# Optimization experiments

Hardware: AMD Instinct MI355X
Metric: run time of the kernel (lower is better)

## Reference

```python
import jax, jax.numpy as jnp
from jax import lax
import numpy as np

DN = ('NHWC', 'HWIO', 'NHWC')  # NHWC activations, HWIO kernels (TF layout)
EPS = 1e-3


def setup_inputs() -> dict:
    key = jax.random.key(0)
    ks = jax.random.split(key, 6)
    B, H, W, C = 16, 64, 64, 256
    x = jax.random.normal(ks[0], (B, H, W, C), jnp.float32)
    # per-sample predicted kernels (scaled to keep activations well-conditioned)
    depthwise_kernels = jax.random.normal(ks[1], (B, 3, 3, C, C), jnp.float32) * 0.02
    pointwise_kernels = jax.random.normal(ks[2], (B, 1, 1, C, C), jnp.float32) * 0.06
    biases = jax.random.normal(ks[3], (B, C), jnp.float32) * 0.1
    # shared trailing Conv2D layer params
    conv_w = jax.random.normal(ks[4], (3, 3, C, C), jnp.float32) * 0.02
    conv_b = jnp.zeros((C,), jnp.float32)
    return dict(x=x, depthwise_kernels=depthwise_kernels,
                pointwise_kernels=pointwise_kernels, biases=biases,
                conv_w=conv_w, conv_b=conv_b)


def _instance_norm(x):
    # tf.nn.moments over spatial dims (population variance), eps=0.001
    mean = jnp.mean(x, axis=(1, 2), keepdims=True)
    var = jnp.var(x, axis=(1, 2), keepdims=True)
    return (x - mean) * lax.rsqrt(var + EPS)


def _reflect_pad_hw(x, p=1):
    pad = [(0, 0)] * (x.ndim - 3) + [(p, p), (p, p), (0, 0)]
    return jnp.pad(x, pad, mode='reflect')


def _per_sample_conv(xi, dk, pk, bi):
    # xi: [H,W,C]; dk: [3,3,C,Cm]; pk: [1,1,Cm,Co]; bi: [Co]
    xp = _reflect_pad_hw(xi)[None]  # [1,H+2,W+2,C]
    y = lax.conv_general_dilated(xp, dk, (1, 1), 'VALID', dimension_numbers=DN)
    y = lax.conv_general_dilated(y, pk, (1, 1), 'VALID', dimension_numbers=DN)
    return (y + bi)[0]


def reference(x, depthwise_kernels, pointwise_kernels, biases, conv_w, conv_b):
    x = _instance_norm(x)
    # per-sample kernels -> vmap over batch (replaces tf.map_fn)
    x = jax.vmap(_per_sample_conv)(x, depthwise_kernels, pointwise_kernels, biases)
    # shared Conv2D: reflect pad + VALID conv + bias
    xp = _reflect_pad_hw(x)
    y = lax.conv_general_dilated(xp, conv_w, (1, 1), 'VALID', dimension_numbers=DN)
    return y + conv_b
```

## Files before the change

kernel.cpp:

```cpp
#include <hip/hip_runtime.h>


typedef __bf16 bf16x8 __attribute__((ext_vector_type(8)));
typedef float f32x4 __attribute__((ext_vector_type(4)));

__device__ __forceinline__ float bf2f(unsigned short v) {
    return __uint_as_float(((unsigned int)v) << 16);
}
__device__ __forceinline__ unsigned short f2bf(float f) {
    unsigned int u = __float_as_uint(f);
    unsigned int r = (u + 0x7FFFu + ((u >> 16) & 1u)) >> 16;
    return (unsigned short)r;
}
__device__ __forceinline__ float ldg_elem(const void* p, size_t idx, bool isbf) {
    return isbf ? bf2f(((const unsigned short*)p)[idx]) : ((const float*)p)[idx];
}

__device__ __forceinline__ void gload16(const void* g, void* l) {
    __builtin_amdgcn_global_load_lds(
        (__attribute__((address_space(1))) void*)(unsigned long long)g,
        (__attribute__((address_space(3))) void*)(unsigned long long)l,
        16, 0, 0);
}

#define RAW_BARRIER() do { asm volatile("" ::: "memory"); \
                           __builtin_amdgcn_s_barrier();   \
                           asm volatile("" ::: "memory"); } while (0)

__global__ void detect_dtype(const unsigned short* __restrict__ x, int* __restrict__ flag) {
    __shared__ int wild;
    if (threadIdx.x == 0) wild = 0;
    __syncthreads();
    int cnt = 0;
    for (int i = 0; i < 16; ++i) {
        float a = fabsf(bf2f(x[threadIdx.x * 16 + i]));
        if (!(a < 64.f) || (a != 0.f && a < 1e-5f)) cnt++;
    }
    atomicAdd(&wild, cnt);
    __syncthreads();
    if (threadIdx.x == 0) *flag = (wild > 512) ? 0 : 1;
}

__global__ void norm_partial2(const void* __restrict__ x, const int* __restrict__ flag,
                              float* __restrict__ partS, float* __restrict__ partQ) {
    const bool isbf = (*flag != 0);
    const int b = blockIdx.x, ch = blockIdx.y;
    const int t = threadIdx.x;
    const int l = t & 63;
    const int c4 = l * 4;
    const int sp0 = t >> 6;
    const size_t base = ((size_t)(b * 4096 + ch * 128 + sp0)) * 256 + c4;
    float s[4] = {0.f, 0.f, 0.f, 0.f}, q[4] = {0.f, 0.f, 0.f, 0.f};
    if (isbf) {
        for (int i = 0; i < 32; ++i) {
            const unsigned short* p = (const unsigned short*)x + base + (size_t)i * 1024;
            ushort4 v = *(const ushort4*)p;
            float a[4] = {bf2f(v.x), bf2f(v.y), bf2f(v.z), bf2f(v.w)};
#pragma unroll
            for (int j = 0; j < 4; ++j) { s[j] += a[j]; q[j] += a[j] * a[j]; }
        }
    } else {
        for (int i = 0; i < 32; ++i) {
            float4 v = *(const float4*)((const float*)x + base + (size_t)i * 1024);
            float a[4] = {v.x, v.y, v.z, v.w};
#pragma unroll
            for (int j = 0; j < 4; ++j) { s[j] += a[j]; q[j] += a[j] * a[j]; }
        }
    }
    __shared__ float red[4][64][9];
#pragma unroll
    for (int j = 0; j < 4; ++j) { red[sp0][l][j] = s[j]; red[sp0][l][4 + j] = q[j]; }
    __syncthreads();
    if (t < 64) {
#pragma unroll
        for (int j = 0; j < 4; ++j) {
            float ss = red[0][t][j] + red[1][t][j] + red[2][t][j] + red[3][t][j];
            float qq = red[0][t][4 + j] + red[1][t][4 + j] + red[2][t][4 + j] + red[3][t][4 + j];
            int c = t * 4 + j;
            partS[(b * 32 + ch) * 256 + c] = ss;
            partQ[(b * 32 + ch) * 256 + c] = qq;
        }
    }
}

__global__ void norm_finalize2(const float* __restrict__ partS, const float* __restrict__ partQ,
                               float* __restrict__ mean, float* __restrict__ rstd) {
    const int b = blockIdx.x, c = threadIdx.x;
    float s = 0.f, q = 0.f;
    for (int k = 0; k < 32; ++k) {
        s += partS[(b * 32 + k) * 256 + c];
        q += partQ[(b * 32 + k) * 256 + c];
    }
    float m = s * (1.f / 4096.f);
    float v = q * (1.f / 4096.f) - m * m;
    mean[b * 256 + c] = m;
    rstd[b * 256 + c] = rsqrtf(v + 1e-3f);
}

__global__ void norm_apply(const void* __restrict__ x, const int* __restrict__ flag,
                           const float* __restrict__ mean, const float* __restrict__ rstd,
                           unsigned short* __restrict__ xn) {
    const bool isbf = (*flag != 0);
    size_t e = ((size_t)blockIdx.x * 256 + threadIdx.x) * 8;
    int c0 = (int)(e & 255);
    int bc = (int)(e >> 20) * 256 + c0;
    float v[8];
    if (isbf) {
        uint4 raw = *(const uint4*)((const unsigned short*)x + e);
        unsigned int rr[4] = {raw.x, raw.y, raw.z, raw.w};
#pragma unroll
        for (int i = 0; i < 4; ++i) {
            v[2 * i]     = bf2f((unsigned short)(rr[i] & 0xFFFF));
            v[2 * i + 1] = bf2f((unsigned short)(rr[i] >> 16));
        }
    } else {
        float4 f0 = *(const float4*)((const float*)x + e);
        float4 f1 = *(const float4*)((const float*)x + e + 4);
        v[0] = f0.x; v[1] = f0.y; v[2] = f0.z; v[3] = f0.w;
        v[4] = f1.x; v[5] = f1.y; v[6] = f1.z; v[7] = f1.w;
    }
    unsigned int o[4];
#pragma unroll
    for (int i = 0; i < 4; ++i) {
        unsigned short lo = f2bf((v[2 * i]     - mean[bc + 2 * i])     * rstd[bc + 2 * i]);
        unsigned short hi = f2bf((v[2 * i + 1] - mean[bc + 2 * i + 1]) * rstd[bc + 2 * i + 1]);
        o[i] = (unsigned int)lo | ((unsigned int)hi << 16);
    }
    uint4 out; out.x = o[0]; out.y = o[1]; out.z = o[2]; out.w = o[3];
    *(uint4*)(xn + e) = out;
}

template <bool SCALE>
__global__ void transpose_wk(const void* __restrict__ src, const int* __restrict__ flag,
                             unsigned short* __restrict__ dst,
                             int s_per, long dstBStride, int coStride,
                             const float* __restrict__ rstd) {
    __shared__ unsigned short tile[64][66];
    const bool isbf = (*flag != 0);
    const int sl = blockIdx.x;
    const int b = sl / s_per;
    const size_t dbase = (size_t)b * (size_t)dstBStride + (size_t)(sl % s_per) * 256;
    const int ci0 = blockIdx.y * 64, co0 = blockIdx.z * 64;
    const int t = threadIdx.x;
    const int co4 = (t & 15) * 4;
    const int r0 = t >> 4;
#pragma unroll
    for (int i = 0; i < 4; ++i) {
        int r = r0 + i * 16;
        size_t sidx = (size_t)sl * 65536 + (size_t)(ci0 + r) * 256 + co0 + co4;
        if (isbf) {
            ushort4 v = *(const ushort4*)((const unsigned short*)src + sidx);
            tile[r][co4] = v.x; tile[r][co4 + 1] = v.y;
            tile[r][co4 + 2] = v.z; tile[r][co4 + 3] = v.w;
        } else {
            float4 v = *(const float4*)((const float*)src + sidx);
            tile[r][co4] = f2bf(v.x); tile[r][co4 + 1] = f2bf(v.y);
            tile[r][co4 + 2] = f2bf(v.z); tile[r][co4 + 3] = f2bf(v.w);
        }
    }
    __syncthreads();
    const int cip = (t & 31) * 2;
    const int cob = t >> 5;
    float s0 = 1.f, s1 = 1.f;
    if (SCALE) { s0 = rstd[b * 256 + ci0 + cip]; s1 = rstd[b * 256 + ci0 + cip + 1]; }
#pragma unroll
    for (int i = 0; i < 8; ++i) {
        int co = cob + i * 8;
        unsigned short lo = tile[cip][co], hi = tile[cip + 1][co];
        if (SCALE) { lo = f2bf(bf2f(lo) * s0); hi = f2bf(bf2f(hi) * s1); }
        *(unsigned int*)(dst + dbase + (size_t)(co0 + co) * coStride + ci0 + cip) =
            (unsigned int)lo | ((unsigned int)hi << 16);
    }
}

__global__ void corr_kernel(const unsigned short* __restrict__ dkT,
                            const float* __restrict__ mean,
                            float* __restrict__ negcorr) {
    const int b = blockIdx.x;
    const int lane = threadIdx.x & 63;
    const int co = blockIdx.y * 4 + (threadIdx.x >> 6);
    const unsigned short* wp = dkT + (size_t)(b * 256 + co) * 2304;
    const float* mb = mean + b * 256;
    const int ci0 = (lane & 31) * 8;
    float4 ma = *(const float4*)(mb + ci0);
    float4 mc = *(const float4*)(mb + ci0 + 4);
    float mm[8] = {ma.x, ma.y, ma.z, ma.w, mc.x, mc.y, mc.z, mc.w};
    float sum = 0.f;
#pragma unroll
    for (int c = 0; c < 5; ++c) {
        int k = c * 512 + lane * 8;
        if (k < 2304) {
            uint4 w = *(const uint4*)(wp + k);
            unsigned int wsv[4] = {w.x, w.y, w.z, w.w};
#pragma unroll
            for (int j = 0; j < 4; ++j) {
                sum += bf2f((unsigned short)(wsv[j] & 0xFFFF)) * mm[2 * j];
                sum += bf2f((unsigned short)(wsv[j] >> 16)) * mm[2 * j + 1];
            }
        }
    }
#pragma unroll
    for (int off = 32; off > 0; off >>= 1) sum += __shfl_down(sum, off);
    if (lane == 0) negcorr[b * 256 + co] = -sum;
}

template <bool PER_SAMPLE_W, int BIAS_MODE, bool OUT_F32>
__global__ __launch_bounds__(512, 2) void conv3x3_256(const unsigned short* __restrict__ src,
                                                      const int* __restrict__ flag,
                                                      const unsigned short* __restrict__ wT,
                                                      const void* __restrict__ bias,
                                                      void* __restrict__ dst) {
    constexpr int KTOT = 2304;
    extern __shared__ unsigned short smem[];

    const int t = threadIdx.x;
    const int lane = t & 63;
    const int wave = t >> 6;
    const int wr = wave >> 1;
    const int wc = wave & 1;
    const int bid = blockIdx.x + 16 * blockIdx.z;
    const int b  = (bid & 7) + ((bid >> 3) & 1) * 8;
    const int mt = bid >> 4;
    const int m0 = mt * 256;
    const int R0 = mt * 4;
    const unsigned short* srcB = src + (size_t)b * (4096 * 256);
    const unsigned short* wB = wT + (PER_SAMPLE_W ? (size_t)b * 256 * KTOT : (size_t)0);
    const bool in_bf = (BIAS_MODE >= 2) ? (*flag != 0) : true;

    const int wx = t >> 3;
    const int wg = ((t & 7) ^ (wx & 7)) << 3;
    int wrow[6];
#pragma unroll
    for (int u = 0; u < 6; ++u) {
        int r = R0 - 1 + u;
        wrow[u] = (r < 0) ? 1 : (r > 63 ? 62 : r);
    }
    const unsigned short* winsrc[6];
#pragma unroll
    for (int u = 0; u < 6; ++u)
        winsrc[u] = srcB + ((size_t)wrow[u] * 64 + wx) * 256 + wg;
    const unsigned short* bsrc = wB + (size_t)wx * KTOT + wg;

    auto issueB2 = [&](int T, int u0) {
        const int koff = (T % 9) * 256 + (T / 9) * 64;
        unsigned short* bdst = smem + 24576 + (T % 3) * 16384 + wave * 512;
        gload16(bsrc + (size_t)u0 * 64 * KTOT + koff, bdst + u0 * 4096);
        gload16(bsrc + (size_t)(u0 + 1) * 64 * KTOT + koff, bdst + (u0 + 1) * 4096);
    };

    f32x4 acc[4][8];
#pragma unroll
    for (int i = 0; i < 4; ++i)
#pragma unroll
        for (int j = 0; j < 8; ++j) acc[i][j] = (f32x4){0.f, 0.f, 0.f, 0.f};

    const int fr = lane & 15;
    const int quad = lane >> 4;
    const int cn = wc * 128;

    auto readB = [&](int jn, int n) -> bf16x8 {
        const int T = jn >> 1, h = jn & 1;
        const int co = cn + n * 16 + fr;
        const unsigned short* p = smem + 24576 + (T % 3) * 16384 + co * 64
                                  + ((((h << 2) + quad) ^ (co & 7)) << 3);
        return *(const bf16x8*)p;
    };
    auto readA = [&](int jn, int mi) -> bf16x8 {
        const int T = jn >> 1, h = jn & 1;
        const int tap = T % 9;
        const int dh = tap / 3 - 1, dw = tap % 3 - 1;
        int ww = mi * 16 + fr + dw;
        ww = (ww < 0) ? 1 : (ww > 63 ? 62 : ww);
        const unsigned short* p = smem + (wr + 1 + dh) * 4096 + ww * 64
                                  + ((((h << 2) + quad) ^ (ww & 7)) << 3);
        return *(const bf16x8*)p;
    };

#pragma unroll
    for (int u = 0; u < 6; ++u)
        gload16(winsrc[u], smem + u * 4096 + wave * 512);
    issueB2(0, 0); issueB2(0, 2);
    issueB2(1, 0); issueB2(1, 2);
    asm volatile("s_waitcnt vmcnt(0)" ::: "memory");
    RAW_BARRIER();

    bf16x8 afc[4], bfc[8];
#pragma unroll
    for (int mi = 0; mi < 4; ++mi) afc[mi] = readA(0, mi);
#pragma unroll
    for (int n = 0; n < 8; ++n) bfc[n] = readB(0, n);

    for (int j = 0; j < 72; ++j) {
        const int T = j >> 1, h = j & 1;
        const int scj = j % 18;

        if (scj == 0 && j > 0) {
            const int cgo = (j / 18) * 64;
#pragma unroll
            for (int u = 0; u < 6; ++u)
                gload16(winsrc[u] + cgo, smem + u * 4096 + wave * 512);
            asm volatile("s_waitcnt vmcnt(0)" ::: "memory");
            RAW_BARRIER();
#pragma unroll
            for (int mi = 0; mi < 4; ++mi) afc[mi] = readA(j, mi);
        }

        if (T + 2 < 36) issueB2(T + 2, h * 2);

        __builtin_amdgcn_s_setprio(1);
#pragma unroll
        for (int mi = 0; mi < 4; ++mi)
#pragma unroll
            for (int n = 0; n < 8; ++n)
                acc[mi][n] = __builtin_amdgcn_mfma_f32_16x16x32_bf16(afc[mi], bfc[n], acc[mi][n], 0, 0, 0);
        __builtin_amdgcn_s_setprio(0);

        if (j < 71) {
#pragma unroll
            for (int n = 0; n < 8; ++n) bfc[n] = readB(j + 1, n);
            if ((j + 1) % 18 != 0) {
#pragma unroll
                for (int mi = 0; mi < 4; ++mi) afc[mi] = readA(j + 1, mi);
            }
        }

        asm volatile("s_waitcnt vmcnt(0)" ::: "memory");
        RAW_BARRIER();
    }

    const int rbase = quad * 4;
    float bv[8];
#pragma unroll
    for (int n = 0; n < 8; ++n) {
        int nn = cn + n * 16 + fr;
        if (BIAS_MODE == 2)      bv[n] = ldg_elem(bias, b * 256 + nn, in_bf);
        else if (BIAS_MODE == 3) bv[n] = ldg_elem(bias, nn, in_bf);
        else                     bv[n] = 0.f;
    }
#pragma unroll
    for (int m = 0; m < 4; ++m) {
#pragma unroll
        for (int rr = 0; rr < 4; ++rr) {
            int mm = m0 + wr * 64 + m * 16 + rbase + rr;
            size_t rowoff = ((size_t)b * 4096 + mm) * 256;
#pragma unroll
            for (int n = 0; n < 8; ++n) {
                int nn = cn + n * 16 + fr;
                float val = acc[m][n][rr] + bv[n];
                if (OUT_F32) ((float*)dst)[rowoff + nn] = val;
                else         ((unsigned short*)dst)[rowoff + nn] = f2bf(val);
            }
        }
    }
}

template <int KSLICES, bool PER_SAMPLE_W, int BIAS_MODE, bool IS3X3, bool OUT_F32>
__global__ __launch_bounds__(512, 2) void gemm_conv_256(const unsigned short* __restrict__ src,
                                                        const int* __restrict__ flag,
                                                        const unsigned short* __restrict__ wT,
                                                        const void* __restrict__ bias,
                                                        void* __restrict__ dst) {
    constexpr int KTOT = KSLICES * 256;
    constexpr int NKT = KTOT / 64;
    static_assert(NKT >= 2, "pipeline needs >=2 K-tiles");
    extern __shared__ unsigned short smem[];

    const int t = threadIdx.x;
    const int lane = t & 63;
    const int wave = t >> 6;
    const int wr = wave >> 2;
    const int wc = wave & 3;
    const int bid = blockIdx.x + 16 * blockIdx.z;
    const int b  = (bid & 7) + ((bid >> 3) & 1) * 8;
    const int m0 = (bid >> 4) * 256;
    const unsigned short* srcB = src + (size_t)b * (4096 * 256);
    const unsigned short* wB = wT + (PER_SAMPLE_W ? (size_t)b * 256 * KTOT : (size_t)0);
    const bool in_bf = (BIAS_MODE >= 2) ? (*flag != 0) : true;

    const int trow = t >> 3;
    const int tswz = ((t & 7) ^ (trow & 7)) << 3;
    int hU[4], wU[4];
#pragma unroll
    for (int u = 0; u < 4; ++u) {
        int m = m0 + u * 64 + trow;
        hU[u] = m >> 6; wU[u] = m & 63;
    }
    const unsigned short* gBu[4];
#pragma unroll
    for (int u = 0; u < 4; ++u)
        gBu[u] = wB + (size_t)(u * 64 + trow) * KTOT + tswz;

    f32x4 acc[8][4];
#pragma unroll
    for (int i = 0; i < 8; ++i)
#pragma unroll
        for (int j = 0; j < 4; ++j) acc[i][j] = (f32x4){0.f, 0.f, 0.f, 0.f};

    const int fr = lane & 15;
    const int quad = lane >> 4;
    const int fsw = fr & 7;
    const int ks0 = ((quad) ^ fsw) << 3;
    const int ks1 = ((quad + 4) ^ fsw) << 3;
    const int rm = wr * 128;
    const int cn = wc * 64;

#pragma unroll
    for (int kt = 0; kt < 2; ++kt) {
        const int pdh = IS3X3 ? -1 : 0;
        const int pdw = IS3X3 ? -1 : 0;
        const int pchb = (kt & 3) << 6;
        unsigned short* ldsAW = smem + kt * 32768 + wave * 512;
#pragma unroll
        for (int u = 0; u < 4; ++u) {
            int hh = hU[u] + pdh; hh = (hh < 0) ? 1 : (hh > 63 ? 62 : hh);
            int ww = wU[u] + pdw; ww = (ww < 0) ? 1 : (ww > 63 ? 62 : ww);
            gload16(srcB + (size_t)((hh << 6) + ww) * 256 + pchb + tswz, ldsAW + u * 4096);
        }
#pragma unroll
        for (int u = 0; u < 4; ++u)
            gload16(gBu[u] + (size_t)kt * 64, ldsAW + 16384 + u * 4096);
    }
    asm volatile("s_waitcnt vmcnt(8)" ::: "memory");
    RAW_BARRIER();

    bf16x8 af[4][2], bfr[4][2];
    size_t aoff[4];
    int cur_s = -1;

    for (int i = 0; i < NKT; ++i) {
        const int buf = i & 1;
        const unsigned short* As_b = smem + buf * 32768;
        const unsigned short* Bs_b = As_b + 16384;
        unsigned short* ldsAW = smem + buf * 32768 + wave * 512;
        const int kt2 = i + 2;
        const bool st = (kt2 < NKT);

#pragma unroll
        for (int m = 0; m < 4; ++m) {
            const unsigned short* rp = As_b + (rm + m * 16 + fr) * 64;
            af[m][0] = *(const bf16x8*)(rp + ks0);
            af[m][1] = *(const bf16x8*)(rp + ks1);
        }
#pragma unroll
        for (int n = 0; n < 2; ++n) {
            const unsigned short* rp = Bs_b + (cn + n * 16 + fr) * 64;
            bfr[n][0] = *(const bf16x8*)(rp + ks0);
            bfr[n][1] = *(const bf16x8*)(rp + ks1);
        }
        __builtin_amdgcn_s_setprio(1);
#pragma unroll
        for (int m = 0; m < 4; ++m)
#pragma unroll
            for (int n = 0; n < 2; ++n) {
                acc[m][n] = __builtin_amdgcn_mfma_f32_16x16x32_bf16(af[m][0], bfr[n][0], acc[m][n], 0, 0, 0);
                acc[m][n] = __builtin_amdgcn_mfma_f32_16x16x32_bf16(af[m][1], bfr[n][1], acc[m][n], 0, 0, 0);
            }
        __builtin_amdgcn_s_setprio(0);

#pragma unroll
        for (int n = 2; n < 4; ++n) {
            const unsigned short* rp = Bs_b + (cn + n * 16 + fr) * 64;
            bfr[n][0] = *(const bf16x8*)(rp + ks0);
            bfr[n][1] = *(const bf16x8*)(rp + ks1);
        }
        __builtin_amdgcn_s_setprio(1);
#pragma unroll
        for (int m = 0; m < 4; ++m)
#pragma unroll
            for (int n = 2; n < 4; ++n) {
                acc[m][n] = __builtin_amdgcn_mfma_f32_16x16x32_bf16(af[m][0], bfr[n][0], acc[m][n], 0, 0, 0);
                acc[m][n] = __builtin_amdgcn_mfma_f32_16x16x32_bf16(af[m][1], bfr[n][1], acc[m][n], 0, 0, 0);
            }
        __builtin_amdgcn_s_setprio(0);

#pragma unroll
        for (int m = 0; m < 4; ++m) {
            const unsigned short* rp = As_b + (rm + 64 + m * 16 + fr) * 64;
            af[m][0] = *(const bf16x8*)(rp + ks0);
            af[m][1] = *(const bf16x8*)(rp + ks1);
        }
        __builtin_amdgcn_s_setprio(1);
#pragma unroll
        for (int m = 0; m < 4; ++m)
#pragma unroll
            for (int n = 0; n < 4; ++n) {
                acc[4 + m][n] = __builtin_amdgcn_mfma_f32_16x16x32_bf16(af[m][0], bfr[n][0], acc[4 + m][n], 0, 0, 0);
                acc[4 + m][n] = __builtin_amdgcn_mfma_f32_16x16x32_bf16(af[m][1], bfr[n][1], acc[4 + m][n], 0, 0, 0);
            }
        __builtin_amdgcn_s_setprio(0);

        RAW_BARRIER();
        if (st) {
            if (IS3X3) {
                const int s2 = kt2 >> 2;
                if (s2 != cur_s) {
                    cur_s = s2;
                    const int dh2 = s2 / 3 - 1, dw2 = s2 % 3 - 1;
#pragma unroll
                    for (int u = 0; u < 4; ++u) {
                        int hh = hU[u] + dh2; hh = (hh < 0) ? 1 : (hh > 63 ? 62 : hh);
                        int ww = wU[u] + dw2; ww = (ww < 0) ? 1 : (ww > 63 ? 62 : ww);
                        aoff[u] = (size_t)((hh << 6) + ww) * 256 + tswz;
                    }
                }
            } else if (cur_s < 0) {
                cur_s = 0;
#pragma unroll
                for (int u = 0; u < 4; ++u)
                    aoff[u] = (size_t)((hU[u] << 6) + wU[u]) * 256 + tswz;
            }
            const int chb2 = (kt2 & 3) << 6;
#pragma unroll
            for (int u = 0; u < 4; ++u)
                gload16(srcB + aoff[u] + chb2, ldsAW + u * 4096);
#pragma unroll
            for (int u = 0; u < 4; ++u)
                gload16(gBu[u] + (size_t)kt2 * 64, ldsAW + 16384 + u * 4096);
            asm volatile("s_waitcnt vmcnt(8)" ::: "memory");
        } else if (i + 1 < NKT) {
            asm volatile("s_waitcnt vmcnt(0)" ::: "memory");
        }
        RAW_BARRIER();
    }

    const int rbase = quad * 4;
    float bv[4];
#pragma unroll
    for (int n = 0; n < 4; ++n) {
        int nn = cn + n * 16 + fr;
        if (BIAS_MODE == 2)      bv[n] = ldg_elem(bias, b * 256 + nn, in_bf);
        else if (BIAS_MODE == 3) bv[n] = ldg_elem(bias, nn, in_bf);
        else                     bv[n] = 0.f;
    }
#pragma unroll
    for (int m = 0; m < 8; ++m) {
#pragma unroll
        for (int rr = 0; rr < 4; ++rr) {
            int mm = m0 + rm + m * 16 + rbase + rr;
            size_t rowoff = ((size_t)b * 4096 + mm) * 256;
#pragma unroll
            for (int n = 0; n < 4; ++n) {
                int nn = cn + n * 16 + fr;
                float val = acc[m][n][rr] + bv[n];
                if (OUT_F32) ((float*)dst)[rowoff + nn] = val;
                else         ((unsigned short*)dst)[rowoff + nn] = f2bf(val);
            }
        }
    }
}

template <int KSLICES, bool PER_SAMPLE_W, int BIAS_MODE, bool IS3X3, bool SRC_ADAPT, bool OUT_F32>
__global__ __launch_bounds__(256) void gemm_conv(const void* __restrict__ src,
                                                 const int* __restrict__ flag,
                                                 const unsigned short* __restrict__ wT,
                                                 const void* __restrict__ bias,
                                                 void* __restrict__ dst) {
    constexpr int KTOT = KSLICES * 256;
    __shared__ unsigned short As[128][40];
    __shared__ unsigned short Bs[128][40];

    const bool in_bf = (SRC_ADAPT || BIAS_MODE >= 2) ? (*flag != 0) : true;
    const int t = threadIdx.x;
    const int b = blockIdx.z;
    const int m0 = blockIdx.x * 128;
    const int n0 = blockIdx.y * 128;
    const size_t srcOfs = (size_t)b * (4096 * 256);
    const unsigned short* wB = wT + (PER_SAMPLE_W ? (size_t)b * 256 * KTOT : (size_t)0);

    f32x4 acc[4][4];
#pragma unroll
    for (int i = 0; i < 4; ++i)
#pragma unroll
        for (int j = 0; j < 4; ++j) acc[i][j] = (f32x4){0.f, 0.f, 0.f, 0.f};

    const int lane = t & 63;
    const int wave = t >> 6;
    const int rm = (wave >> 1) * 64;
    const int cn = (wave & 1) * 64;
    const int fr = lane & 15;
    const int kg = (lane >> 4) * 8;

    for (int kk = 0; kk < KTOT / 32; ++kk) {
        const int k0 = kk * 32;
        const int s = k0 >> 8;
        const int ci0 = k0 & 255;
        const int dh = IS3X3 ? (s / 3) - 1 : 0;
        const int dw = IS3X3 ? (s % 3) - 1 : 0;
        __syncthreads();
#pragma unroll
        for (int cc = 0; cc < 2; ++cc) {
            int ch = t + cc * 256;
            int r = ch >> 2;
            int ko = (ch & 3) << 3;
            int m = m0 + r;
            int h = m >> 6, w = m & 63;
            if (IS3X3) {
                h += dh; h = (h < 0) ? 1 : (h > 63 ? 62 : h);
                w += dw; w = (w < 0) ? 1 : (w > 63 ? 62 : w);
            }
            size_t eidx = srcOfs + (size_t)((h << 6) + w) * 256 + ci0 + ko;
            if (!SRC_ADAPT || in_bf) {
                uint4 v = *(const uint4*)((const unsigned short*)src + eidx);
                *(uint4*)&As[r][ko] = v;
            } else {
                const float* sf = (const float*)src + eidx;
                float4 f0 = *(const float4*)sf;
                float4 f1 = *(const float4*)(sf + 4);
                uint4 v;
                v.x = (unsigned int)f2bf(f0.x) | ((unsigned int)f2bf(f0.y) << 16);
                v.y = (unsigned int)f2bf(f0.z) | ((unsigned int)f2bf(f0.w) << 16);
                v.z = (unsigned int)f2bf(f1.x) | ((unsigned int)f2bf(f1.y) << 16);
                v.w = (unsigned int)f2bf(f1.z) | ((unsigned int)f2bf(f1.w) << 16);
                *(uint4*)&As[r][ko] = v;
            }
        }
#pragma unroll
        for (int cc = 0; cc < 2; ++cc) {
            int ch = t + cc * 256;
            int n = ch >> 2;
            int ko = (ch & 3) << 3;
            uint4 v = *(const uint4*)(wB + (size_t)(n0 + n) * KTOT + k0 + ko);
            *(uint4*)&Bs[n][ko] = v;
        }
        __syncthreads();

        bf16x8 af[4], bfr[4];
#pragma unroll
        for (int i = 0; i < 4; ++i) af[i] = *(const bf16x8*)&As[rm + i * 16 + fr][kg];
#pragma unroll
        for (int j = 0; j < 4; ++j) bfr[j] = *(const bf16x8*)&Bs[cn + j * 16 + fr][kg];
#pragma unroll
        for (int i = 0; i < 4; ++i)
#pragma unroll
            for (int j = 0; j < 4; ++j)
                acc[i][j] = __builtin_amdgcn_mfma_f32_16x16x32_bf16(af[i], bfr[j], acc[i][j], 0, 0, 0);
    }

    const int rbase = (lane >> 4) * 4;
    const int col = lane & 15;
    float bv[4];
#pragma unroll
    for (int j = 0; j < 4; ++j) {
        int n = n0 + cn + j * 16 + col;
        if (BIAS_MODE == 1)      bv[j] = ((const float*)bias)[b * 256 + n];
        else if (BIAS_MODE == 2) bv[j] = ldg_elem(bias, b * 256 + n, in_bf);
        else if (BIAS_MODE == 3) bv[j] = ldg_elem(bias, n, in_bf);
        else                     bv[j] = 0.f;
    }
#pragma unroll
    for (int i = 0; i < 4; ++i) {
#pragma unroll
        for (int rr = 0; rr < 4; ++rr) {
            int m = m0 + rm + i * 16 + rbase + rr;
            size_t rowoff = ((size_t)b * 4096 + m) * 256;
#pragma unroll
            for (int j = 0; j < 4; ++j) {
                int n = n0 + cn + j * 16 + col;
                float val = acc[i][j][rr] + bv[j];
                if (OUT_F32) ((float*)dst)[rowoff + n] = val;
                else         ((unsigned short*)dst)[rowoff + n] = f2bf(val);
            }
        }
    }
}

extern "C" void kernel_launch(void* const* d_in, const int* in_sizes, int n_in,
                              void* d_out, int out_size, void* d_ws, size_t ws_size,
                              hipStream_t stream) {
    const void* x    = d_in[0];
    const void* dk   = d_in[1];
    const void* pk   = d_in[2];
    const void* bias = d_in[3];
    const void* cw   = d_in[4];
    const void* cb   = d_in[5];

    const size_t NEED_SMALL = 36896768u;
    const size_t NEED_BIG   = 55771136u;
    if (ws_size < NEED_SMALL) return;
    const bool big = (ws_size >= NEED_BIG);

    char* ws = (char*)d_ws;
    int*   flagp   = (int*)ws;
    float* meanp   = (float*)(ws + 1024);
    float* rstdp   = (float*)(ws + 17408);
    float* negcorr = (float*)(ws + 33792);
    unsigned short* pkT = (unsigned short*)(ws + 65536);
    unsigned short* cwT = (unsigned short*)(ws + 2162688);
    unsigned short* dkT = (unsigned short*)(ws + 3342336);
    unsigned short* xn  = (unsigned short*)(ws + 22216704);
    float* partS = (float*)(ws + 22216704);
    float* partQ = (float*)(ws + 22216704 + 524288);
    unsigned short* y2  = big ? xn : dkT;
    unsigned short* y1  = (unsigned short*)d_out;

    hipFuncSetAttribute(reinterpret_cast<const void*>(conv3x3_256<true, 0, false>),
                        hipFuncAttributeMaxDynamicSharedMemorySize, 147456);
    hipFuncSetAttribute(reinterpret_cast<const void*>(conv3x3_256<false, 3, true>),
                        hipFuncAttributeMaxDynamicSharedMemorySize, 147456);
    hipFuncSetAttribute(reinterpret_cast<const void*>(gemm_conv_256<1, true, 2, false, false>),
                        hipFuncAttributeMaxDynamicSharedMemorySize, 131072);

    detect_dtype<<<1, 256, 0, stream>>>((const unsigned short*)x, flagp);
    norm_partial2<<<dim3(16, 32), 256, 0, stream>>>(x, flagp, partS, partQ);
    norm_finalize2<<<16, 256, 0, stream>>>(partS, partQ, meanp, rstdp);

    transpose_wk<false><<<dim3(16, 4, 4), 256, 0, stream>>>(pk, flagp, pkT, 1, 65536L, 256, nullptr);
    transpose_wk<false><<<dim3(9, 4, 4), 256, 0, stream>>>(cw, flagp, cwT, 9, 0L, 2304, nullptr);

    if (big) {
        transpose_wk<false><<<dim3(144, 4, 4), 256, 0, stream>>>(dk, flagp, dkT, 9, 589824L, 2304, nullptr);
        norm_apply<<<8192, 256, 0, stream>>>(x, flagp, meanp, rstdp, xn);
        conv3x3_256<true, 0, false><<<dim3(16, 1, 16), 512, 147456, stream>>>(xn, flagp, dkT, nullptr, y1);
    } else {
        transpose_wk<true><<<dim3(144, 4, 4), 256, 0, stream>>>(dk, flagp, dkT, 9, 589824L, 2304, rstdp);
        corr_kernel<<<dim3(16, 64), 256, 0, stream>>>(dkT, meanp, negcorr);
        gemm_conv<9, true, 1, true, true, false><<<dim3(32, 2, 16), 256, 0, stream>>>(x, flagp, dkT, negcorr, y1);
    }

    gemm_conv_256<1, true, 2, false, false><<<dim3(16, 1, 16), 512, 131072, stream>>>(y1, flagp, pkT, bias, y2);
    conv3x3_256<false, 3, true><<<dim3(16, 1, 16), 512, 147456, stream>>>(y2, flagp, cwT, cb, d_out);
}
```

Measured before the change: 353.1 us.

## Split 3x3 conv output channels across two blocks to raise occupancy

```diff
diff --git a/kernel.cpp b/kernel.cpp
--- a/kernel.cpp
+++ b/kernel.cpp
@@ -205,11 +205,11 @@
 }
 
 template <bool PER_SAMPLE_W, int BIAS_MODE, bool OUT_F32>
-__global__ __launch_bounds__(512, 2) void conv3x3_256(const unsigned short* __restrict__ src,
-                                                      const int* __restrict__ flag,
-                                                      const unsigned short* __restrict__ wT,
-                                                      const void* __restrict__ bias,
-                                                      void* __restrict__ dst) {
+__global__ __launch_bounds__(512, 4) void conv3x3_w(const unsigned short* __restrict__ src,
+                                                    const int* __restrict__ flag,
+                                                    const unsigned short* __restrict__ wT,
+                                                    const void* __restrict__ bias,
+                                                    void* __restrict__ dst) {
     constexpr int KTOT = 2304;
     extern __shared__ unsigned short smem[];
 
@@ -223,6 +223,7 @@
     const int mt = bid >> 4;
     const int m0 = mt * 256;
     const int R0 = mt * 4;
+    const int n0 = blockIdx.y * 128;
     const unsigned short* srcB = src + (size_t)b * (4096 * 256);
     const unsigned short* wB = wT + (PER_SAMPLE_W ? (size_t)b * 256 * KTOT : (size_t)0);
     const bool in_bf = (BIAS_MODE >= 2) ? (*flag != 0) : true;
@@ -239,100 +240,86 @@
 #pragma unroll
     for (int u = 0; u < 6; ++u)
         winsrc[u] = srcB + ((size_t)wrow[u] * 64 + wx) * 256 + wg;
-    const unsigned short* bsrc = wB + (size_t)wx * KTOT + wg;
-
-    auto issueB2 = [&](int T, int u0) {
+    const unsigned short* bsrc = wB + (size_t)(n0 + wx) * KTOT + wg;
+
+    auto issueB = [&](int T) {
         const int koff = (T % 9) * 256 + (T / 9) * 64;
-        unsigned short* bdst = smem + 24576 + (T % 3) * 16384 + wave * 512;
-        gload16(bsrc + (size_t)u0 * 64 * KTOT + koff, bdst + u0 * 4096);
-        gload16(bsrc + (size_t)(u0 + 1) * 64 * KTOT + koff, bdst + (u0 + 1) * 4096);
+        unsigned short* bdst = smem + 24576 + (T & 1) * 8192 + wave * 512;
+        gload16(bsrc + koff, bdst);
+        gload16(bsrc + (size_t)64 * KTOT + koff, bdst + 4096);
     };
 
-    f32x4 acc[4][8];
+    f32x4 acc[4][4];
 #pragma unroll
     for (int i = 0; i < 4; ++i)
 #pragma unroll
-        for (int j = 0; j < 8; ++j) acc[i][j] = (f32x4){0.f, 0.f, 0.f, 0.f};
+        for (int j = 0; j < 4; ++j) acc[i][j] = (f32x4){0.f, 0.f, 0.f, 0.f};
 
     const int fr = lane & 15;
     const int quad = lane >> 4;
-    const int cn = wc * 128;
-
-    auto readB = [&](int jn, int n) -> bf16x8 {
-        const int T = jn >> 1, h = jn & 1;
-        const int co = cn + n * 16 + fr;
-        const unsigned short* p = smem + 24576 + (T % 3) * 16384 + co * 64
-                                  + ((((h << 2) + quad) ^ (co & 7)) << 3);
-        return *(const bf16x8*)p;
-    };
-    auto readA = [&](int jn, int mi) -> bf16x8 {
-        const int T = jn >> 1, h = jn & 1;
-        const int tap = T % 9;
-        const int dh = tap / 3 - 1, dw = tap % 3 - 1;
-        int ww = mi * 16 + fr + dw;
-        ww = (ww < 0) ? 1 : (ww > 63 ? 62 : ww);
-        const unsigned short* p = smem + (wr + 1 + dh) * 4096 + ww * 64
-                                  + ((((h << 2) + quad) ^ (ww & 7)) << 3);
-        return *(const bf16x8*)p;
-    };
+    const int cnw = wc * 64;
 
 #pragma unroll
     for (int u = 0; u < 6; ++u)
         gload16(winsrc[u], smem + u * 4096 + wave * 512);
-    issueB2(0, 0); issueB2(0, 2);
-    issueB2(1, 0); issueB2(1, 2);
-    asm volatile("s_waitcnt vmcnt(0)" ::: "memory");
-    RAW_BARRIER();
-
-    bf16x8 afc[4], bfc[8];
-#pragma unroll
-    for (int mi = 0; mi < 4; ++mi) afc[mi] = readA(0, mi);
-#pragma unroll
-    for (int n = 0; n < 8; ++n) bfc[n] = readB(0, n);
-
-    for (int j = 0; j < 72; ++j) {
-        const int T = j >> 1, h = j & 1;
-        const int scj = j % 18;
-
-        if (scj == 0 && j > 0) {
-            const int cgo = (j / 18) * 64;
+    issueB(0);
+
+    bf16x8 af[4], bf[4];
+
+    for (int T = 0; T < 36; ++T) {
+        const int cg = T / 9, tap = T % 9;
+        const int dh = tap / 3 - 1, dw = tap % 3 - 1;
+
+        if (tap == 0 && T > 0) {
+            asm volatile("s_waitcnt vmcnt(0)" ::: "memory");
+            RAW_BARRIER();
+            const int cgo = cg * 64;
 #pragma unroll
             for (int u = 0; u < 6; ++u)
                 gload16(winsrc[u] + cgo, smem + u * 4096 + wave * 512);
             asm volatile("s_waitcnt vmcnt(0)" ::: "memory");
             RAW_BARRIER();
-#pragma unroll
-            for (int mi = 0; mi < 4; ++mi) afc[mi] = readA(j, mi);
-        }
-
-        if (T + 2 < 36) issueB2(T + 2, h * 2);
-
-        __builtin_amdgcn_s_setprio(1);
-#pragma unroll
-        for (int mi = 0; mi < 4; ++mi)
-#pragma unroll
-            for (int n = 0; n < 8; ++n)
-                acc[mi][n] = __builtin_amdgcn_mfma_f32_16x16x32_bf16(afc[mi], bfc[n], acc[mi][n], 0, 0, 0);
-        __builtin_amdgcn_s_setprio(0);
-
-        if (j < 71) {
-#pragma unroll
-            for (int n = 0; n < 8; ++n) bfc[n] = readB(j + 1, n);
-            if ((j + 1) % 18 != 0) {
-#pragma unroll
-                for (int mi = 0; mi < 4; ++mi) afc[mi] = readA(j + 1, mi);
-            }
-        }
-
-        asm volatile("s_waitcnt vmcnt(0)" ::: "memory");
-        RAW_BARRIER();
+        } else {
+            asm volatile("s_waitcnt vmcnt(0)" ::: "memory");
+            RAW_BARRIER();
+        }
+        if (T + 1 < 36) issueB(T + 1);
+
+        const unsigned short* Arow = smem + (wr + 1 + dh) * 4096;
+        const unsigned short* Bb = smem + 24576 + (T & 1) * 8192;
+        int aww[4];
+#pragma unroll
+        for (int mi = 0; mi < 4; ++mi) {
+            int ww = mi * 16 + fr + dw;
+            aww[mi] = (ww < 0) ? 1 : (ww > 63 ? 62 : ww);
+        }
+
+#pragma unroll
+        for (int h = 0; h < 2; ++h) {
+            const int kq = (h << 2) + quad;
+#pragma unroll
+            for (int mi = 0; mi < 4; ++mi)
+                af[mi] = *(const bf16x8*)(Arow + aww[mi] * 64 + ((kq ^ (aww[mi] & 7)) << 3));
+#pragma unroll
+            for (int n = 0; n < 4; ++n) {
+                const int co = cnw + n * 16 + fr;
+                bf[n] = *(const bf16x8*)(Bb + co * 64 + ((kq ^ (co & 7)) << 3));
+            }
+            __builtin_amdgcn_s_setprio(1);
+#pragma unroll
+            for (int mi = 0; mi < 4; ++mi)
+#pragma unroll
+                for (int n = 0; n < 4; ++n)
+                    acc[mi][n] = __builtin_amdgcn_mfma_f32_16x16x32_bf16(af[mi], bf[n], acc[mi][n], 0, 0, 0);
+            __builtin_amdgcn_s_setprio(0);
+        }
     }
 
     const int rbase = quad * 4;
-    float bv[8];
-#pragma unroll
-    for (int n = 0; n < 8; ++n) {
-        int nn = cn + n * 16 + fr;
+    float bv[4];
+#pragma unroll
+    for (int n = 0; n < 4; ++n) {
+        int nn = n0 + cnw + n * 16 + fr;
         if (BIAS_MODE == 2)      bv[n] = ldg_elem(bias, b * 256 + nn, in_bf);
         else if (BIAS_MODE == 3) bv[n] = ldg_elem(bias, nn, in_bf);
         else                     bv[n] = 0.f;
@@ -344,8 +331,8 @@
             int mm = m0 + wr * 64 + m * 16 + rbase + rr;
             size_t rowoff = ((size_t)b * 4096 + mm) * 256;
 #pragma unroll
-            for (int n = 0; n < 8; ++n) {
-                int nn = cn + n * 16 + fr;
+            for (int n = 0; n < 4; ++n) {
+                int nn = n0 + cnw + n * 16 + fr;
                 float val = acc[m][n][rr] + bv[n];
                 if (OUT_F32) ((float*)dst)[rowoff + nn] = val;
                 else         ((unsigned short*)dst)[rowoff + nn] = f2bf(val);
@@ -406,14 +393,15 @@
 
 #pragma unroll
     for (int kt = 0; kt < 2; ++kt) {
-        const int pdh = IS3X3 ? -1 : 0;
-        const int pdw = IS3X3 ? -1 : 0;
         const int pchb = (kt & 3) << 6;
         unsigned short* ldsAW = smem + kt * 32768 + wave * 512;
 #pragma unroll
         for (int u = 0; u < 4; ++u) {
-            int hh = hU[u] + pdh; hh = (hh < 0) ? 1 : (hh > 63 ? 62 : hh);
-            int ww = wU[u] + pdw; ww = (ww < 0) ? 1 : (ww > 63 ? 62 : ww);
+            int hh = hU[u]; int ww = wU[u];
+            if (IS3X3) {
+                hh -= 1; hh = (hh < 0) ? 1 : (hh > 63 ? 62 : hh);
+                ww -= 1; ww = (ww < 0) ? 1 : (ww > 63 ? 62 : ww);
+            }
             gload16(srcB + (size_t)((hh << 6) + ww) * 256 + pchb + tswz, ldsAW + u * 4096);
         }
 #pragma unroll
@@ -491,19 +479,7 @@
 
         RAW_BARRIER();
         if (st) {
-            if (IS3X3) {
-                const int s2 = kt2 >> 2;
-                if (s2 != cur_s) {
-                    cur_s = s2;
-                    const int dh2 = s2 / 3 - 1, dw2 = s2 % 3 - 1;
-#pragma unroll
-                    for (int u = 0; u < 4; ++u) {
-                        int hh = hU[u] + dh2; hh = (hh < 0) ? 1 : (hh > 63 ? 62 : hh);
-                        int ww = wU[u] + dw2; ww = (ww < 0) ? 1 : (ww > 63 ? 62 : ww);
-                        aoff[u] = (size_t)((hh << 6) + ww) * 256 + tswz;
-                    }
-                }
-            } else if (cur_s < 0) {
+            if (cur_s < 0) {
                 cur_s = 0;
 #pragma unroll
                 for (int u = 0; u < 4; ++u)
@@ -693,10 +669,10 @@
     unsigned short* y2  = big ? xn : dkT;
     unsigned short* y1  = (unsigned short*)d_out;
 
-    hipFuncSetAttribute(reinterpret_cast<const void*>(conv3x3_256<true, 0, false>),
-                        hipFuncAttributeMaxDynamicSharedMemorySize, 147456);
-    hipFuncSetAttribute(reinterpret_cast<const void*>(conv3x3_256<false, 3, true>),
-                        hipFuncAttributeMaxDynamicSharedMemorySize, 147456);
+    hipFuncSetAttribute(reinterpret_cast<const void*>(conv3x3_w<true, 0, false>),
+                        hipFuncAttributeMaxDynamicSharedMemorySize, 81920);
+    hipFuncSetAttribute(reinterpret_cast<const void*>(conv3x3_w<false, 3, true>),
+                        hipFuncAttributeMaxDynamicSharedMemorySize, 81920);
     hipFuncSetAttribute(reinterpret_cast<const void*>(gemm_conv_256<1, true, 2, false, false>),
                         hipFuncAttributeMaxDynamicSharedMemorySize, 131072);
 
@@ -710,7 +686,7 @@
     if (big) {
         transpose_wk<false><<<dim3(144, 4, 4), 256, 0, stream>>>(dk, flagp, dkT, 9, 589824L, 2304, nullptr);
         norm_apply<<<8192, 256, 0, stream>>>(x, flagp, meanp, rstdp, xn);
-        conv3x3_256<true, 0, false><<<dim3(16, 1, 16), 512, 147456, stream>>>(xn, flagp, dkT, nullptr, y1);
+        conv3x3_w<true, 0, false><<<dim3(16, 2, 16), 512, 81920, stream>>>(xn, flagp, dkT, nullptr, y1);
     } else {
         transpose_wk<true><<<dim3(144, 4, 4), 256, 0, stream>>>(dk, flagp, dkT, 9, 589824L, 2304, rstdp);
         corr_kernel<<<dim3(16, 64), 256, 0, stream>>>(dkT, meanp, negcorr);
@@ -718,5 +694,5 @@
     }
 
     gemm_conv_256<1, true, 2, false, false><<<dim3(16, 1, 16), 512, 131072, stream>>>(y1, flagp, pkT, bias, y2);
-    conv3x3_256<false, 3, true><<<dim3(16, 1, 16), 512, 147456, stream>>>(y2, flagp, cwT, cb, d_out);
-}
+    conv3x3_w<false, 3, true><<<dim3(16, 2, 16), 512, 81920, stream>>>(y2, flagp, cwT, cb, d_out);
+}
```

Result: no change. 346.4 us (-1.9%).
